# Kernel optimization log

Hardware: AMD Instinct MI355X
Metric: run time of the kernel (lower is better)

The kernel has to match this reference:

```python
import jax, jax.numpy as jnp
import numpy as np

N_NODES = 50000


def gcn_conv(x, W, b, src, dst, ew, n):
    """PyG-style GCNConv: D^-1/2 (A+I) D^-1/2 X W + b with self-loops of weight 1."""
    h = x @ W                                   # [N, out]
    loop = jnp.arange(n, dtype=src.dtype)
    s = jnp.concatenate([src, loop])            # [E+N]
    d = jnp.concatenate([dst, loop])
    w = jnp.concatenate([ew, jnp.ones((n,), dtype=x.dtype)])
    deg = jax.ops.segment_sum(w, d, num_segments=n)
    dinv = jnp.where(deg > 0, jax.lax.rsqrt(deg), 0.0)
    norm = dinv[s] * w * dinv[d]                # [E+N]
    out = jax.ops.segment_sum(h[s] * norm[:, None], d, num_segments=n)
    return out + b


def setup_inputs() -> dict:
    key = jax.random.key(0)
    ks = jax.random.split(key, 12)
    in_feats, hidden = 128, 128
    half = hidden // 2
    E = 800000
    x = jax.random.normal(ks[0], (N_NODES, in_feats), dtype=jnp.float32)
    edge_index = jax.random.randint(ks[1], (2, E), 0, N_NODES, dtype=jnp.int64)
    edge_weight = jax.random.uniform(ks[2], (E,), dtype=jnp.float32)
    def lin(k, fan_in, shape):
        bound = 1.0 / np.sqrt(fan_in)
        return jax.random.uniform(k, shape, minval=-bound, maxval=bound, dtype=jnp.float32)
    return {
        "x": x,
        "edge_index": edge_index,
        "edge_weight": edge_weight,
        "W1": lin(ks[3], in_feats, (in_feats, hidden)),
        "b1": jnp.zeros((hidden,), jnp.float32),
        "W2": lin(ks[4], hidden, (hidden, hidden)),
        "b2": jnp.zeros((hidden,), jnp.float32),
        "Ws": lin(ks[5], in_feats, (in_feats, hidden)),
        "bs": lin(ks[6], in_feats, (hidden,)),
        "Wl": lin(ks[7], in_feats, (in_feats, half)),
        "bl": jnp.zeros((half,), jnp.float32),
        "Wl2": lin(ks[8], half, (half, 1)),
        "bl2": lin(ks[9], half, (1,)),
    }


def reference(x, edge_index, edge_weight, W1, b1, W2, b2, Ws, bs, Wl, bl, Wl2, bl2):
    n = x.shape[0]
    src, dst = edge_index[0], edge_index[1]
    # conv1 + ReLU over neighbors
    h_neighbors = jax.nn.relu(gcn_conv(x, W1, b1, src, dst, edge_weight, n))
    # leader score: GCNConv -> ReLU -> Linear(.,1) -> sigmoid, per node
    ls_h = jax.nn.relu(gcn_conv(x, Wl, bl, src, dst, edge_weight, n))
    leader_score = jax.nn.sigmoid(ls_h @ Wl2 + bl2)        # [N, 1]
    # gated fusion of self projection vs neighbor aggregation
    h_self_proj = x @ Ws + bs
    h_new = (1.0 - leader_score) * h_neighbors + leader_score * h_self_proj
    h_final = jax.nn.relu(gcn_conv(h_new, W2, b2, src, dst, edge_weight, n))
    return (h_final, leader_score)
```

## Files before the change

kernel.cpp:

```cpp
#include <hip/hip_runtime.h>
#include <math.h>

#define THREADS 256
#define ELLS 96
#define GEMM_YSTRIDE 104
#define NPHA 256
#define BSHIFT 7
#define NBMAX 392
#define BCAP 2560

typedef unsigned int uint32;
typedef unsigned long long ull64;
typedef __attribute__((ext_vector_type(8))) short bf16x8;
typedef __attribute__((ext_vector_type(4))) float f32x4;
typedef __attribute__((ext_vector_type(2))) float f32x2;

__device__ __forceinline__ unsigned short f2bf_rne(float x) {
  uint32 u = __float_as_uint(x);
  u += 0x7fffu + ((u >> 16) & 1u);
  return (unsigned short)(u >> 16);
}

__device__ __forceinline__ f32x2 dw2f2(uint32 d) {
  f32x2 r;
  r.x = __uint_as_float(d << 16);
  r.y = __uint_as_float(d & 0xffff0000u);
  return r;
}


__global__ __launch_bounds__(256) void prep_fused(ull64* __restrict__ packed, uint32* __restrict__ gcnt, int n,
                                                  const float* __restrict__ W1, const float* __restrict__ Wl,
                                                  const float* __restrict__ Ws, const float* __restrict__ W2,
                                                  unsigned short* __restrict__ whi, unsigned short* __restrict__ wlo,
                                                  const float* __restrict__ x, unsigned short* __restrict__ xraw,
                                                  int nInit, int nW) {
  int b = blockIdx.x;
  int t = threadIdx.x;
  if (b < nInit) {
    int i = b * 256 + t;
    if (i < n) packed[i] = 0ull;
    if (i < NBMAX) gcnt[i] = 0u;
  } else if (b < nInit + nW) {
    int idx = (b - nInit) * 256 + t;
    if (idx >= 448 * 128) return;
    int slot = idx >> 7;
    int k = idx & 127;
    const float* W; int ncol, ncols;
    if (slot < 128)      { W = W1; ncol = slot;       ncols = 128; }
    else if (slot < 192) { W = Wl; ncol = slot - 128; ncols = 64;  }
    else if (slot < 320) { W = Ws; ncol = slot - 192; ncols = 128; }
    else                 { W = W2; ncol = slot - 320; ncols = 128; }
    float v = W[(size_t)k * ncols + ncol];
    unsigned short hi = f2bf_rne(v);
    float hif = __uint_as_float((uint32)hi << 16);
    unsigned short lo = f2bf_rne(v - hif);
    whi[idx] = hi;
    wlo[idx] = lo;
  } else {
    int i = (b - nInit - nW) * 256 + t;
    if (i >= n * 16) return;
    const float* px = x + (size_t)i * 8;
    float4 a = *(const float4*)px;
    float4 c = *(const float4*)(px + 4);
    ushort4 r0, r1;
    r0.x = f2bf_rne(a.x); r0.y = f2bf_rne(a.y); r0.z = f2bf_rne(a.z); r0.w = f2bf_rne(a.w);
    r1.x = f2bf_rne(c.x); r1.y = f2bf_rne(c.y); r1.z = f2bf_rne(c.z); r1.w = f2bf_rne(c.w);
    *(ushort4*)(xraw + (size_t)i * 8) = r0;
    *(ushort4*)(xraw + (size_t)i * 8 + 4) = r1;
  }
}


struct Chunk {
  const unsigned short* A;
  const unsigned short* whi;
  const unsigned short* wlo;
  const float* bias;
  void* out;
  int ostride;
  int obf16;
};
struct GemmArgs { Chunk c[5]; };

__device__ __forceinline__ void gemm_body(const Chunk& d, int M, int nTiles, int tile0, int tstride) {
  const unsigned short* A = d.A;
  int w = threadIdx.x >> 6, lane = threadIdx.x & 63;
  int n16 = lane & 15, quad = lane >> 4;

  bf16x8 Bh[4][4], Bl[4][4];
  {
    const unsigned short* wh = d.whi + (size_t)n16 * 128 + quad * 8;
    const unsigned short* wl = d.wlo + (size_t)n16 * 128 + quad * 8;
#pragma unroll
    for (int ct = 0; ct < 4; ct++)
#pragma unroll
      for (int ks = 0; ks < 4; ks++) {
        Bh[ct][ks] = *(const bf16x8*)(wh + ct * 16 * 128 + ks * 32);
        Bl[ct][ks] = *(const bf16x8*)(wl + ct * 16 * 128 + ks * 32);
      }
  }
  float bv[4];
#pragma unroll
  for (int ct = 0; ct < 4; ct++) bv[ct] = d.bias ? d.bias[ct * 16 + n16] : 0.f;

  int tile = tile0;
  bf16x8 av0[4], av1[4];
  if (tile < nTiles) {
    int bm = tile * 128;
    int r0 = bm + w * 32 + n16, r1 = r0 + 16;
    int r0c = r0 < M ? r0 : M - 1;
    int r1c = r1 < M ? r1 : M - 1;
    const unsigned short* a0 = A + (size_t)r0c * 128 + quad * 8;
    const unsigned short* a1 = A + (size_t)r1c * 128 + quad * 8;
#pragma unroll
    for (int ks = 0; ks < 4; ks++) {
      av0[ks] = *(const bf16x8*)(a0 + ks * 32);
      av1[ks] = *(const bf16x8*)(a1 + ks * 32);
    }
  }

  for (; tile < nTiles; tile += tstride) {
    int nxt = tile + tstride;
    bf16x8 nv0[4], nv1[4];
    if (nxt < nTiles) {
      int bm = nxt * 128;
      int r0 = bm + w * 32 + n16, r1 = r0 + 16;
      int r0c = r0 < M ? r0 : M - 1;
      int r1c = r1 < M ? r1 : M - 1;
      const unsigned short* a0 = A + (size_t)r0c * 128 + quad * 8;
      const unsigned short* a1 = A + (size_t)r1c * 128 + quad * 8;
#pragma unroll
      for (int ks = 0; ks < 4; ks++) {
        nv0[ks] = *(const bf16x8*)(a0 + ks * 32);
        nv1[ks] = *(const bf16x8*)(a1 + ks * 32);
      }
    }

    f32x4 acc[2][4];
#pragma unroll
    for (int rt = 0; rt < 2; rt++)
#pragma unroll
      for (int ct = 0; ct < 4; ct++) acc[rt][ct] = (f32x4){0.f, 0.f, 0.f, 0.f};

#pragma unroll
    for (int ks = 0; ks < 4; ks++)
#pragma unroll
      for (int ct = 0; ct < 4; ct++) {
        acc[0][ct] = __builtin_amdgcn_mfma_f32_16x16x32_bf16(av0[ks], Bh[ct][ks], acc[0][ct], 0, 0, 0);
        acc[0][ct] = __builtin_amdgcn_mfma_f32_16x16x32_bf16(av0[ks], Bl[ct][ks], acc[0][ct], 0, 0, 0);
        acc[1][ct] = __builtin_amdgcn_mfma_f32_16x16x32_bf16(av1[ks], Bh[ct][ks], acc[1][ct], 0, 0, 0);
        acc[1][ct] = __builtin_amdgcn_mfma_f32_16x16x32_bf16(av1[ks], Bl[ct][ks], acc[1][ct], 0, 0, 0);
      }

    int bm = tile * 128;
#pragma unroll
    for (int ct = 0; ct < 4; ct++) {
      int col = ct * 16 + n16;
#pragma unroll
      for (int rt = 0; rt < 2; rt++) {
#pragma unroll
        for (int reg = 0; reg < 4; reg++) {
          int row = bm + w * 32 + rt * 16 + quad * 4 + reg;
          if (row < M) {
            float v = acc[rt][ct][reg] + bv[ct];
            if (d.obf16)
              ((unsigned short*)d.out)[(size_t)row * d.ostride + col] = f2bf_rne(v);
            else
              ((float*)d.out)[(size_t)row * d.ostride + col] = v;
          }
        }
      }
    }

#pragma unroll
    for (int ks = 0; ks < 4; ks++) { av0[ks] = nv0[ks]; av1[ks] = nv1[ks]; }
  }
}

__global__ __launch_bounds__(256, 2) void gemm_v3(GemmArgs args, int M, int nTiles) {
  gemm_body(args.c[blockIdx.x], M, nTiles, blockIdx.y, gridDim.y);
}


__global__ __launch_bounds__(256, 2) void fused_sg(GemmArgs args, int M, int nTiles, int nGemm,
                                                   const int* __restrict__ ei, const float* __restrict__ ew,
                                                   uint32* __restrict__ gcnt, uint2* __restrict__ staging, int E) {
  __shared__ uint32 cntS[NBMAX], curS[NBMAX], gbS[NBMAX];
  int b = blockIdx.x;
  int gemmIdx = -1, phIdx = -1;
  int twice = NPHA * 2;
  if (b < twice) {
    if (b & 1) gemmIdx = b >> 1; else phIdx = b >> 1;
  } else {
    gemmIdx = NPHA + (b - twice);
  }

  if (phIdx >= 0) {
    int t = threadIdx.x;
    int per = (E + NPHA - 1) / NPHA;
    int start = phIdx * per;
    int end = start + per; if (end > E) end = E;
    for (int k = t; k < NBMAX; k += 256) cntS[k] = 0u;
    __syncthreads();
    for (int i = start + t; i < end; i += 256)
      atomicAdd(&cntS[(uint32)ei[E + i] >> BSHIFT], 1u);
    __syncthreads();
    for (int k = t; k < NBMAX; k += 256) {
      uint32 c = cntS[k];
      gbS[k] = c ? atomicAdd(&gcnt[k], c) : 0u;
      curS[k] = 0u;
    }
    __syncthreads();
    for (int i = start + t; i < end; i += 256) {
      int d = ei[E + i];
      int s = ei[i];
      float w = ew[i];
      int bk = d >> BSHIFT;
      uint32 pos = atomicAdd(&curS[bk], 1u) + gbS[bk];
      if (pos < BCAP)
        staging[(size_t)bk * BCAP + pos] = make_uint2(((uint32)(d & 127) << 24) | (uint32)s, __float_as_uint(w));
    }
    return;
  }

  int chunkId = gemmIdx % 5;
  int ytile = gemmIdx / 5;
  gemm_body(args.c[chunkId], M, nTiles, ytile, GEMM_YSTRIDE);
}


__global__ __launch_bounds__(256) void phaseB_kernel(const uint2* __restrict__ staging,
                                                     const uint32* __restrict__ gcnt,
                                                     ull64* __restrict__ packed, int2* __restrict__ ell,
                                                     float* __restrict__ dinv, int* __restrict__ cnt32, int n) {
  int b = blockIdx.x;
  int t = threadIdx.x;
  uint32 cnt = gcnt[b]; if (cnt > BCAP) cnt = BCAP;
  const uint2* sb = staging + (size_t)b * BCAP;
  int dbase = b << BSHIFT;
  for (uint32 i = t; i < cnt; i += 256) {
    uint2 en = sb[i];
    int d = dbase + (int)(en.x >> 24);
    int s = (int)(en.x & 0xffffffu);
    float w = __uint_as_float(en.y);
    uint32 fx = (uint32)(w * 8388608.0f + 0.5f);
    ull64 old = atomicAdd(packed + d, (1ull << 32) | (ull64)fx);
    int slot = (int)(old >> 32);
    if (slot < ELLS)
      ell[(size_t)d * ELLS + slot] = make_int2(s, __float_as_int(w));
  }
  __syncthreads();
  const float S = 1.1920928955078125e-7f;
  int dend = dbase + 128; if (dend > n) dend = n;
  for (int d = dbase + t; d < dend; d += 256) {
    ull64 p = atomicAdd(packed + d, 0ull);
    dinv[d] = rsqrtf(1.0f + (float)(uint32)(p & 0xffffffffull) * S);
    cnt32[d] = (int)(p >> 32);
  }
}


__global__ __launch_bounds__(256) void conv1_fused(const unsigned short* __restrict__ h1,
                                                   const unsigned short* __restrict__ hl,
                                                   const int* __restrict__ cnt,
                                                   const int2* __restrict__ csr,
                                                   const float* __restrict__ dinv,
                                                   const float* __restrict__ b1, const float* __restrict__ bl,
                                                   const float* __restrict__ Wl2, const float* __restrict__ bl2,
                                                   const unsigned short* __restrict__ hself,
                                                   unsigned short* __restrict__ hnew_out,
                                                   float* __restrict__ leader_out, int nnodes) {
  int wave = threadIdx.x >> 6;
  int lane = threadIdx.x & 63;
  int node = blockIdx.x * 4 + wave;
  if (node >= nnodes) return;
  int g = lane >> 4, q = lane & 15;
  bool ql = q < 8;
  int hq = q & 7;
  int rs = node * ELLS;
  int n = cnt[node];
  float di = dinv[node];
  f32x2 dv2 = {di, di};

  f32x2 acc1[4] = {};
  f32x2 accl[4] = {};
  if (g == 0) {
    uint4 v = *(const uint4*)(h1 + (size_t)node * 128 + 8 * q);
    acc1[0] = dv2 * dw2f2(v.x); acc1[1] = dv2 * dw2f2(v.y);
    acc1[2] = dv2 * dw2f2(v.z); acc1[3] = dv2 * dw2f2(v.w);
    if (ql) {
      uint4 vl = *(const uint4*)(hl + (size_t)node * 64 + 8 * q);
      accl[0] = dv2 * dw2f2(vl.x); accl[1] = dv2 * dw2f2(vl.y);
      accl[2] = dv2 * dw2f2(vl.z); accl[3] = dv2 * dw2f2(vl.w);
    }
  }

  int e = g;
  for (; e + 4 < n; e += 8) {
    int2 en0 = csr[rs + e];
    int2 en1 = csr[rs + e + 4];
    float wz0 = __int_as_float(en0.y) * dinv[en0.x];
    float wz1 = __int_as_float(en1.y) * dinv[en1.x];
    f32x2 w0 = {wz0, wz0};
    f32x2 w1 = {wz1, wz1};
    uint4 a0 = *(const uint4*)(h1 + (size_t)en0.x * 128 + 8 * q);
    uint4 a1 = *(const uint4*)(h1 + (size_t)en1.x * 128 + 8 * q);
    int srcl = ql ? en0.x : en1.x;
    float wzl = ql ? wz0 : wz1;
    uint4 c0 = *(const uint4*)(hl + (size_t)srcl * 64 + 8 * hq);
    f32x2 wl2 = {wzl, wzl};
    accl[0] += wl2 * dw2f2(c0.x);
    accl[1] += wl2 * dw2f2(c0.y);
    accl[2] += wl2 * dw2f2(c0.z);
    accl[3] += wl2 * dw2f2(c0.w);
    acc1[0] += w0 * dw2f2(a0.x) + w1 * dw2f2(a1.x);
    acc1[1] += w0 * dw2f2(a0.y) + w1 * dw2f2(a1.y);
    acc1[2] += w0 * dw2f2(a0.z) + w1 * dw2f2(a1.z);
    acc1[3] += w0 * dw2f2(a0.w) + w1 * dw2f2(a1.w);
  }
  if (e < n) {
    int2 en = csr[rs + e];
    float wz0 = __int_as_float(en.y) * dinv[en.x];
    f32x2 w0 = {wz0, wz0};
    uint4 a0 = *(const uint4*)(h1 + (size_t)en.x * 128 + 8 * q);
    float wzl = ql ? wz0 : 0.f;
    uint4 c0 = *(const uint4*)(hl + (size_t)en.x * 64 + 8 * hq);
    f32x2 wl2 = {wzl, wzl};
    accl[0] += wl2 * dw2f2(c0.x);
    accl[1] += wl2 * dw2f2(c0.y);
    accl[2] += wl2 * dw2f2(c0.z);
    accl[3] += wl2 * dw2f2(c0.w);
    acc1[0] += w0 * dw2f2(a0.x);
    acc1[1] += w0 * dw2f2(a0.y);
    acc1[2] += w0 * dw2f2(a0.z);
    acc1[3] += w0 * dw2f2(a0.w);
  }

#pragma unroll
  for (int k = 0; k < 4; k++) {
    acc1[k].x += __shfl_xor(acc1[k].x, 16);
    acc1[k].y += __shfl_xor(acc1[k].y, 16);
    acc1[k].x += __shfl_xor(acc1[k].x, 32);
    acc1[k].y += __shfl_xor(acc1[k].y, 32);
    accl[k].x += __shfl_xor(accl[k].x, 16);
    accl[k].y += __shfl_xor(accl[k].y, 16);
    accl[k].x += __shfl_xor(accl[k].x, 32);
    accl[k].y += __shfl_xor(accl[k].y, 32);
    accl[k].x += __shfl_xor(accl[k].x, 8);
    accl[k].y += __shfl_xor(accl[k].y, 8);
  }

  float part = 0.f;
  if (ql) {
    float b[8], w2[8];
    *(float4*)&b[0] = *(const float4*)(bl + 8 * q);
    *(float4*)&b[4] = *(const float4*)(bl + 8 * q + 4);
    *(float4*)&w2[0] = *(const float4*)(Wl2 + 8 * q);
    *(float4*)&w2[4] = *(const float4*)(Wl2 + 8 * q + 4);
#pragma unroll
    for (int k = 0; k < 4; k++) {
      part += fmaxf(di * accl[k].x + b[2 * k], 0.f) * w2[2 * k];
      part += fmaxf(di * accl[k].y + b[2 * k + 1], 0.f) * w2[2 * k + 1];
    }
  }
  part += __shfl_xor(part, 1);
  part += __shfl_xor(part, 2);
  part += __shfl_xor(part, 4);
  float z = __shfl(part, 0) + bl2[0];
  float l = 1.f / (1.f + expf(-z));
  if (lane == 0) leader_out[node] = l;

  if (g == 0) {
    float b[8], r[8], hs[8];
    *(float4*)&b[0] = *(const float4*)(b1 + 8 * q);
    *(float4*)&b[4] = *(const float4*)(b1 + 8 * q + 4);
    uint4 hsv = *(const uint4*)(hself + (size_t)node * 128 + 8 * q);
    f32x2 h0 = dw2f2(hsv.x), h1v = dw2f2(hsv.y), h2v = dw2f2(hsv.z), h3v = dw2f2(hsv.w);
    hs[0] = h0.x; hs[1] = h0.y; hs[2] = h1v.x; hs[3] = h1v.y;
    hs[4] = h2v.x; hs[5] = h2v.y; hs[6] = h3v.x; hs[7] = h3v.y;
    float a[8];
    a[0] = acc1[0].x; a[1] = acc1[0].y; a[2] = acc1[1].x; a[3] = acc1[1].y;
    a[4] = acc1[2].x; a[5] = acc1[2].y; a[6] = acc1[3].x; a[7] = acc1[3].y;
#pragma unroll
    for (int j = 0; j < 8; j++) {
      r[j] = fmaxf(di * a[j] + b[j], 0.f);
      r[j] = (1.f - l) * r[j] + l * hs[j];
      r[j] *= di;
    }
    ushort4 p0, p1;
    p0.x = f2bf_rne(r[0]); p0.y = f2bf_rne(r[1]); p0.z = f2bf_rne(r[2]); p0.w = f2bf_rne(r[3]);
    p1.x = f2bf_rne(r[4]); p1.y = f2bf_rne(r[5]); p1.z = f2bf_rne(r[6]); p1.w = f2bf_rne(r[7]);
    *(ushort4*)(hnew_out + (size_t)node * 128 + 8 * q) = p0;
    *(ushort4*)(hnew_out + (size_t)node * 128 + 8 * q + 4) = p1;
  }
}


__global__ __launch_bounds__(256) void agg_conv2_kernel(const unsigned short* __restrict__ h,
                                                        const int* __restrict__ cnt,
                                                        const int2* __restrict__ csr,
                                                        const float* __restrict__ dinv, const float* __restrict__ bias,
                                                        float* __restrict__ out, int nnodes) {
  int wave = threadIdx.x >> 6;
  int lane = threadIdx.x & 63;
  int node = blockIdx.x * 4 + wave;
  if (node >= nnodes) return;
  int g = lane >> 4;
  int q = lane & 15;
  int rs = node * ELLS;
  int n = cnt[node];
  float di = dinv[node];

  f32x2 acc[4] = {};
  if (g == 0) {
    uint4 v = *(const uint4*)(h + (size_t)node * 128 + 8 * q);
    acc[0] = dw2f2(v.x); acc[1] = dw2f2(v.y);
    acc[2] = dw2f2(v.z); acc[3] = dw2f2(v.w);
  }
  int e = g;
  for (; e + 4 < n; e += 8) {
    int2 en0 = csr[rs + e];
    int2 en1 = csr[rs + e + 4];
    f32x2 w0 = {__int_as_float(en0.y), __int_as_float(en0.y)};
    f32x2 w1 = {__int_as_float(en1.y), __int_as_float(en1.y)};
    uint4 v0 = *(const uint4*)(h + (size_t)en0.x * 128 + 8 * q);
    uint4 v1 = *(const uint4*)(h + (size_t)en1.x * 128 + 8 * q);
    acc[0] += w0 * dw2f2(v0.x) + w1 * dw2f2(v1.x);
    acc[1] += w0 * dw2f2(v0.y) + w1 * dw2f2(v1.y);
    acc[2] += w0 * dw2f2(v0.z) + w1 * dw2f2(v1.z);
    acc[3] += w0 * dw2f2(v0.w) + w1 * dw2f2(v1.w);
  }
  if (e < n) {
    int2 en = csr[rs + e];
    f32x2 w0 = {__int_as_float(en.y), __int_as_float(en.y)};
    uint4 v = *(const uint4*)(h + (size_t)en.x * 128 + 8 * q);
    acc[0] += w0 * dw2f2(v.x);
    acc[1] += w0 * dw2f2(v.y);
    acc[2] += w0 * dw2f2(v.z);
    acc[3] += w0 * dw2f2(v.w);
  }
#pragma unroll
  for (int k = 0; k < 4; k++) {
    acc[k].x += __shfl_xor(acc[k].x, 16);
    acc[k].y += __shfl_xor(acc[k].y, 16);
    acc[k].x += __shfl_xor(acc[k].x, 32);
    acc[k].y += __shfl_xor(acc[k].y, 32);
  }
  if (g == 0) {
    float b[8], r[8];
    *(float4*)&b[0] = *(const float4*)(bias + 8 * q);
    *(float4*)&b[4] = *(const float4*)(bias + 8 * q + 4);
    float a[8];
    a[0] = acc[0].x; a[1] = acc[0].y; a[2] = acc[1].x; a[3] = acc[1].y;
    a[4] = acc[2].x; a[5] = acc[2].y; a[6] = acc[3].x; a[7] = acc[3].y;
#pragma unroll
    for (int j = 0; j < 8; j++) r[j] = fmaxf(di * a[j] + b[j], 0.f);
    *(float4*)(out + (size_t)node * 128 + 8 * q) = *(float4*)&r[0];
    *(float4*)(out + (size_t)node * 128 + 8 * q + 4) = *(float4*)&r[4];
  }
}


extern "C" void kernel_launch(void* const* d_in, const int* in_sizes, int n_in,
                              void* d_out, int out_size, void* d_ws, size_t ws_size,
                              hipStream_t stream) {
  const float* x   = (const float*)d_in[0];
  const int*   ei  = (const int*)d_in[1];
  const float* ew  = (const float*)d_in[2];
  const float* W1  = (const float*)d_in[3];
  const float* b1  = (const float*)d_in[4];
  const float* W2  = (const float*)d_in[5];
  const float* b2  = (const float*)d_in[6];
  const float* Wsp = (const float*)d_in[7];
  const float* bs  = (const float*)d_in[8];
  const float* Wl  = (const float*)d_in[9];
  const float* bl  = (const float*)d_in[10];
  const float* Wl2 = (const float*)d_in[11];
  const float* bl2 = (const float*)d_in[12];

  const int N = in_sizes[0] / 128;
  const int E = in_sizes[1] / 2;
  const int NB = (N + 127) >> BSHIFT;

  char* ws = (char*)d_ws;
  size_t off = 0;
  auto alloc = [&](size_t bytes) -> void* {
    void* p = ws + off;
    off = (off + bytes + 255) & ~(size_t)255;
    return p;
  };
  ull64* packed    = (ull64*)alloc((size_t)N * 8);
  uint32* gcnt     = (uint32*)alloc((size_t)NBMAX * 4);
  uint2* staging   = (uint2*)alloc((size_t)NBMAX * BCAP * 8);
  float* dinv      = (float*)alloc((size_t)N * 4);
  int*   cnt32     = (int*)alloc((size_t)N * 4);
  int2*  ell       = (int2*)alloc((size_t)N * ELLS * 8);
  unsigned short* xraw   = (unsigned short*)alloc((size_t)N * 128 * 2);
  unsigned short* h1bf   = (unsigned short*)alloc((size_t)N * 128 * 2);
  unsigned short* hlbf   = (unsigned short*)alloc((size_t)N * 64 * 2);
  unsigned short* hnewbf = (unsigned short*)alloc((size_t)N * 128 * 2);
  unsigned short* hspbf  = (unsigned short*)alloc((size_t)N * 128 * 2);
  unsigned short* whi = (unsigned short*)alloc((size_t)448 * 128 * 2);
  unsigned short* wlo = (unsigned short*)alloc((size_t)448 * 128 * 2);

  float* h_final = (float*)d_out;
  float* leader  = (float*)d_out + (size_t)N * 128;

  int gN = (N + THREADS - 1) / THREADS;
  int gWave = (N + 3) / 4;
  int nTiles = (N + 127) / 128;
  int nCast = (N * 16 + 255) / 256;
  int nW = (448 * 128 + 255) / 256;

  prep_fused<<<gN + nW + nCast, 256, 0, stream>>>(packed, gcnt, N, W1, Wl, Wsp, W2, whi, wlo, x, xraw, gN, nW);

  {
    GemmArgs ga;
    ga.c[0] = {xraw, whi + 0 * 128,   wlo + 0 * 128,   nullptr, h1bf,       128, 1};
    ga.c[1] = {xraw, whi + 64 * 128,  wlo + 64 * 128,  nullptr, h1bf + 64,  128, 1};
    ga.c[2] = {xraw, whi + 128 * 128, wlo + 128 * 128, nullptr, hlbf,       64,  1};
    ga.c[3] = {xraw, whi + 192 * 128, wlo + 192 * 128, bs,      hspbf,      128, 1};
    ga.c[4] = {xraw, whi + 256 * 128, wlo + 256 * 128, bs + 64, hspbf + 64, 128, 1};
    int nGemm = 5 * GEMM_YSTRIDE;
    int totalBlocks = NPHA * 2 + (nGemm - NPHA);
    fused_sg<<<totalBlocks, 256, 0, stream>>>(ga, N, nTiles, nGemm, ei, ew, gcnt, staging, E);
  }

  phaseB_kernel<<<NB, 256, 0, stream>>>(staging, gcnt, packed, ell, dinv, cnt32, N);

  conv1_fused<<<gWave, 256, 0, stream>>>(h1bf, hlbf, cnt32, ell, dinv,
                                         b1, bl, Wl2, bl2, hspbf, hnewbf, leader, N);

  {
    GemmArgs ga;
    ga.c[0] = {hnewbf, whi + 320 * 128, wlo + 320 * 128, nullptr, h1bf,      128, 1};
    ga.c[1] = {hnewbf, whi + 384 * 128, wlo + 384 * 128, nullptr, h1bf + 64, 128, 1};
    ga.c[2] = ga.c[0]; ga.c[3] = ga.c[0]; ga.c[4] = ga.c[0];
    gemm_v3<<<dim3(2, 256), 256, 0, stream>>>(ga, N, nTiles);
  }
  agg_conv2_kernel<<<gWave, 256, 0, stream>>>(h1bf, cnt32, ell,
                                              dinv, b2, h_final, N);
}
```

Measured before the change: 267.9 us.

## Fold input/weight bf16 conversion into GEMMs and use shared-memory degree accumulation

Removes the prep kernel. The GEMM now reads fp32 x directly and converts it to bf16 in registers, and each block builds its bf16 hi/lo weight split itself from the fp32 weights. The phaseB degree and count accumulation moves from global 64-bit atomics on a packed array to per-block shared-memory atomics, and a small memset replaces the rest of the zero-init. This saves one launch and the xraw round trip. In exchange the GEMM reads twice as many bytes for A, and every block does strided scalar weight loads and conversions.

```diff
diff --git a/kernel.cpp b/kernel.cpp
--- a/kernel.cpp
+++ b/kernel.cpp
@@ -28,77 +28,47 @@
   return r;
 }
 
-
-__global__ __launch_bounds__(256) void prep_fused(ull64* __restrict__ packed, uint32* __restrict__ gcnt, int n,
-                                                  const float* __restrict__ W1, const float* __restrict__ Wl,
-                                                  const float* __restrict__ Ws, const float* __restrict__ W2,
-                                                  unsigned short* __restrict__ whi, unsigned short* __restrict__ wlo,
-                                                  const float* __restrict__ x, unsigned short* __restrict__ xraw,
-                                                  int nInit, int nW) {
-  int b = blockIdx.x;
-  int t = threadIdx.x;
-  if (b < nInit) {
-    int i = b * 256 + t;
-    if (i < n) packed[i] = 0ull;
-    if (i < NBMAX) gcnt[i] = 0u;
-  } else if (b < nInit + nW) {
-    int idx = (b - nInit) * 256 + t;
-    if (idx >= 448 * 128) return;
-    int slot = idx >> 7;
-    int k = idx & 127;
-    const float* W; int ncol, ncols;
-    if (slot < 128)      { W = W1; ncol = slot;       ncols = 128; }
-    else if (slot < 192) { W = Wl; ncol = slot - 128; ncols = 64;  }
-    else if (slot < 320) { W = Ws; ncol = slot - 192; ncols = 128; }
-    else                 { W = W2; ncol = slot - 320; ncols = 128; }
-    float v = W[(size_t)k * ncols + ncol];
-    unsigned short hi = f2bf_rne(v);
-    float hif = __uint_as_float((uint32)hi << 16);
-    unsigned short lo = f2bf_rne(v - hif);
-    whi[idx] = hi;
-    wlo[idx] = lo;
-  } else {
-    int i = (b - nInit - nW) * 256 + t;
-    if (i >= n * 16) return;
-    const float* px = x + (size_t)i * 8;
-    float4 a = *(const float4*)px;
-    float4 c = *(const float4*)(px + 4);
-    ushort4 r0, r1;
-    r0.x = f2bf_rne(a.x); r0.y = f2bf_rne(a.y); r0.z = f2bf_rne(a.z); r0.w = f2bf_rne(a.w);
-    r1.x = f2bf_rne(c.x); r1.y = f2bf_rne(c.y); r1.z = f2bf_rne(c.z); r1.w = f2bf_rne(c.w);
-    *(ushort4*)(xraw + (size_t)i * 8) = r0;
-    *(ushort4*)(xraw + (size_t)i * 8 + 4) = r1;
-  }
+__device__ __forceinline__ bf16x8 cvt8(float4 a, float4 b) {
+  bf16x8 r;
+  r[0] = (short)f2bf_rne(a.x); r[1] = (short)f2bf_rne(a.y);
+  r[2] = (short)f2bf_rne(a.z); r[3] = (short)f2bf_rne(a.w);
+  r[4] = (short)f2bf_rne(b.x); r[5] = (short)f2bf_rne(b.y);
+  r[6] = (short)f2bf_rne(b.z); r[7] = (short)f2bf_rne(b.w);
+  return r;
 }
 
 
 struct Chunk {
-  const unsigned short* A;
-  const unsigned short* whi;
-  const unsigned short* wlo;
+  const void* A;
+  const float* W;
+  int wcols;
+  int colbase;
   const float* bias;
   void* out;
   int ostride;
-  int obf16;
 };
 struct GemmArgs { Chunk c[5]; };
 
+template <bool AF32>
 __device__ __forceinline__ void gemm_body(const Chunk& d, int M, int nTiles, int tile0, int tstride) {
-  const unsigned short* A = d.A;
   int w = threadIdx.x >> 6, lane = threadIdx.x & 63;
   int n16 = lane & 15, quad = lane >> 4;
 
   bf16x8 Bh[4][4], Bl[4][4];
   {
-    const unsigned short* wh = d.whi + (size_t)n16 * 128 + quad * 8;
-    const unsigned short* wl = d.wlo + (size_t)n16 * 128 + quad * 8;
+    const float* wb = d.W + d.colbase + n16;
 #pragma unroll
     for (int ct = 0; ct < 4; ct++)
 #pragma unroll
-      for (int ks = 0; ks < 4; ks++) {
-        Bh[ct][ks] = *(const bf16x8*)(wh + ct * 16 * 128 + ks * 32);
-        Bl[ct][ks] = *(const bf16x8*)(wl + ct * 16 * 128 + ks * 32);
-      }
+      for (int ks = 0; ks < 4; ks++)
+#pragma unroll
+        for (int j = 0; j < 8; j++) {
+          float v = wb[(size_t)(quad * 8 + ks * 32 + j) * d.wcols + ct * 16];
+          unsigned short hi = f2bf_rne(v);
+          float hif = __uint_as_float((uint32)hi << 16);
+          Bh[ct][ks][j] = (short)hi;
+          Bl[ct][ks][j] = (short)f2bf_rne(v - hif);
+        }
   }
   float bv[4];
 #pragma unroll
@@ -111,29 +81,53 @@
     int r0 = bm + w * 32 + n16, r1 = r0 + 16;
     int r0c = r0 < M ? r0 : M - 1;
     int r1c = r1 < M ? r1 : M - 1;
-    const unsigned short* a0 = A + (size_t)r0c * 128 + quad * 8;
-    const unsigned short* a1 = A + (size_t)r1c * 128 + quad * 8;
-#pragma unroll
-    for (int ks = 0; ks < 4; ks++) {
-      av0[ks] = *(const bf16x8*)(a0 + ks * 32);
-      av1[ks] = *(const bf16x8*)(a1 + ks * 32);
+    if constexpr (AF32) {
+      const float* a0 = (const float*)d.A + (size_t)r0c * 128 + quad * 8;
+      const float* a1 = (const float*)d.A + (size_t)r1c * 128 + quad * 8;
+#pragma unroll
+      for (int ks = 0; ks < 4; ks++) {
+        av0[ks] = cvt8(*(const float4*)(a0 + ks * 32), *(const float4*)(a0 + ks * 32 + 4));
+        av1[ks] = cvt8(*(const float4*)(a1 + ks * 32), *(const float4*)(a1 + ks * 32 + 4));
+      }
+    } else {
+      const unsigned short* a0 = (const unsigned short*)d.A + (size_t)r0c * 128 + quad * 8;
+      const unsigned short* a1 = (const unsigned short*)d.A + (size_t)r1c * 128 + quad * 8;
+#pragma unroll
+      for (int ks = 0; ks < 4; ks++) {
+        av0[ks] = *(const bf16x8*)(a0 + ks * 32);
+        av1[ks] = *(const bf16x8*)(a1 + ks * 32);
+      }
     }
   }
 
   for (; tile < nTiles; tile += tstride) {
     int nxt = tile + tstride;
+    bool have = (nxt < nTiles);
+    float4 pf0[8], pf1[8];
     bf16x8 nv0[4], nv1[4];
-    if (nxt < nTiles) {
+    if (have) {
       int bm = nxt * 128;
       int r0 = bm + w * 32 + n16, r1 = r0 + 16;
       int r0c = r0 < M ? r0 : M - 1;
       int r1c = r1 < M ? r1 : M - 1;
-      const unsigned short* a0 = A + (size_t)r0c * 128 + quad * 8;
-      const unsigned short* a1 = A + (size_t)r1c * 128 + quad * 8;
-#pragma unroll
-      for (int ks = 0; ks < 4; ks++) {
-        nv0[ks] = *(const bf16x8*)(a0 + ks * 32);
-        nv1[ks] = *(const bf16x8*)(a1 + ks * 32);
+      if constexpr (AF32) {
+        const float* a0 = (const float*)d.A + (size_t)r0c * 128 + quad * 8;
+        const float* a1 = (const float*)d.A + (size_t)r1c * 128 + quad * 8;
+#pragma unroll
+        for (int ks = 0; ks < 4; ks++) {
+          pf0[2 * ks]     = *(const float4*)(a0 + ks * 32);
+          pf0[2 * ks + 1] = *(const float4*)(a0 + ks * 32 + 4);
+          pf1[2 * ks]     = *(const float4*)(a1 + ks * 32);
+          pf1[2 * ks + 1] = *(const float4*)(a1 + ks * 32 + 4);
+        }
+      } else {
+        const unsigned short* a0 = (const unsigned short*)d.A + (size_t)r0c * 128 + quad * 8;
+        const unsigned short* a1 = (const unsigned short*)d.A + (size_t)r1c * 128 + quad * 8;
+#pragma unroll
+        for (int ks = 0; ks < 4; ks++) {
+          nv0[ks] = *(const bf16x8*)(a0 + ks * 32);
+          nv1[ks] = *(const bf16x8*)(a1 + ks * 32);
+        }
       }
     }
 
@@ -164,22 +158,29 @@
           int row = bm + w * 32 + rt * 16 + quad * 4 + reg;
           if (row < M) {
             float v = acc[rt][ct][reg] + bv[ct];
-            if (d.obf16)
-              ((unsigned short*)d.out)[(size_t)row * d.ostride + col] = f2bf_rne(v);
-            else
-              ((float*)d.out)[(size_t)row * d.ostride + col] = v;
+            ((unsigned short*)d.out)[(size_t)row * d.ostride + col] = f2bf_rne(v);
           }
         }
       }
     }
 
-#pragma unroll
-    for (int ks = 0; ks < 4; ks++) { av0[ks] = nv0[ks]; av1[ks] = nv1[ks]; }
+    if (have) {
+      if constexpr (AF32) {
+#pragma unroll
+        for (int ks = 0; ks < 4; ks++) {
+          av0[ks] = cvt8(pf0[2 * ks], pf0[2 * ks + 1]);
+          av1[ks] = cvt8(pf1[2 * ks], pf1[2 * ks + 1]);
+        }
+      } else {
+#pragma unroll
+        for (int ks = 0; ks < 4; ks++) { av0[ks] = nv0[ks]; av1[ks] = nv1[ks]; }
+      }
+    }
   }
 }
 
 __global__ __launch_bounds__(256, 2) void gemm_v3(GemmArgs args, int M, int nTiles) {
-  gemm_body(args.c[blockIdx.x], M, nTiles, blockIdx.y, gridDim.y);
+  gemm_body<false>(args.c[blockIdx.x], M, nTiles, blockIdx.y, gridDim.y);
 }
 
 
@@ -226,37 +227,42 @@
 
   int chunkId = gemmIdx % 5;
   int ytile = gemmIdx / 5;
-  gemm_body(args.c[chunkId], M, nTiles, ytile, GEMM_YSTRIDE);
+  gemm_body<true>(args.c[chunkId], M, nTiles, ytile, GEMM_YSTRIDE);
 }
 
 
 __global__ __launch_bounds__(256) void phaseB_kernel(const uint2* __restrict__ staging,
                                                      const uint32* __restrict__ gcnt,
-                                                     ull64* __restrict__ packed, int2* __restrict__ ell,
+                                                     int2* __restrict__ ell,
                                                      float* __restrict__ dinv, int* __restrict__ cnt32, int n) {
+  __shared__ uint32 cntL[128], sumL[128];
   int b = blockIdx.x;
   int t = threadIdx.x;
+  if (t < 128) { cntL[t] = 0u; sumL[t] = 0u; }
+  __syncthreads();
   uint32 cnt = gcnt[b]; if (cnt > BCAP) cnt = BCAP;
   const uint2* sb = staging + (size_t)b * BCAP;
   int dbase = b << BSHIFT;
   for (uint32 i = t; i < cnt; i += 256) {
     uint2 en = sb[i];
-    int d = dbase + (int)(en.x >> 24);
+    int dl = (int)(en.x >> 24);
     int s = (int)(en.x & 0xffffffu);
     float w = __uint_as_float(en.y);
     uint32 fx = (uint32)(w * 8388608.0f + 0.5f);
-    ull64 old = atomicAdd(packed + d, (1ull << 32) | (ull64)fx);
-    int slot = (int)(old >> 32);
+    atomicAdd(&sumL[dl], fx);
+    uint32 slot = atomicAdd(&cntL[dl], 1u);
     if (slot < ELLS)
-      ell[(size_t)d * ELLS + slot] = make_int2(s, __float_as_int(w));
+      ell[(size_t)(dbase + dl) * ELLS + slot] = make_int2(s, __float_as_int(w));
   }
   __syncthreads();
-  const float S = 1.1920928955078125e-7f;
-  int dend = dbase + 128; if (dend > n) dend = n;
-  for (int d = dbase + t; d < dend; d += 256) {
-    ull64 p = atomicAdd(packed + d, 0ull);
-    dinv[d] = rsqrtf(1.0f + (float)(uint32)(p & 0xffffffffull) * S);
-    cnt32[d] = (int)(p >> 32);
+  if (t < 128) {
+    int d = dbase + t;
+    if (d < n) {
+      const float S = 1.1920928955078125e-7f;
+      dinv[d] = rsqrtf(1.0f + (float)sumL[t] * S);
+      uint32 c = cntL[t];
+      cnt32[d] = (int)(c < ELLS ? c : ELLS);
+    }
   }
 }
 
@@ -490,52 +496,45 @@
     off = (off + bytes + 255) & ~(size_t)255;
     return p;
   };
-  ull64* packed    = (ull64*)alloc((size_t)N * 8);
   uint32* gcnt     = (uint32*)alloc((size_t)NBMAX * 4);
   uint2* staging   = (uint2*)alloc((size_t)NBMAX * BCAP * 8);
   float* dinv      = (float*)alloc((size_t)N * 4);
   int*   cnt32     = (int*)alloc((size_t)N * 4);
   int2*  ell       = (int2*)alloc((size_t)N * ELLS * 8);
-  unsigned short* xraw   = (unsigned short*)alloc((size_t)N * 128 * 2);
   unsigned short* h1bf   = (unsigned short*)alloc((size_t)N * 128 * 2);
   unsigned short* hlbf   = (unsigned short*)alloc((size_t)N * 64 * 2);
   unsigned short* hnewbf = (unsigned short*)alloc((size_t)N * 128 * 2);
   unsigned short* hspbf  = (unsigned short*)alloc((size_t)N * 128 * 2);
-  unsigned short* whi = (unsigned short*)alloc((size_t)448 * 128 * 2);
-  unsigned short* wlo = (unsigned short*)alloc((size_t)448 * 128 * 2);
 
   float* h_final = (float*)d_out;
   float* leader  = (float*)d_out + (size_t)N * 128;
 
-  int gN = (N + THREADS - 1) / THREADS;
   int gWave = (N + 3) / 4;
   int nTiles = (N + 127) / 128;
-  int nCast = (N * 16 + 255) / 256;
-  int nW = (448 * 128 + 255) / 256;
-
-  prep_fused<<<gN + nW + nCast, 256, 0, stream>>>(packed, gcnt, N, W1, Wl, Wsp, W2, whi, wlo, x, xraw, gN, nW);
+
+  hipMemsetAsync(gcnt, 0, (size_t)NBMAX * 4, stream);
 
   {
     GemmArgs ga;
-    ga.c[0] = {xraw, whi + 0 * 128,   wlo + 0 * 128,   nullptr, h1bf,       128, 1};
-    ga.c[1] = {xraw, whi + 64 * 128,  wlo + 64 * 128,  nullptr, h1bf + 64,  128, 1};
-    ga.c[2] = {xraw, whi + 128 * 128, wlo + 128 * 128, nullptr, hlbf,       64,  1};
-    ga.c[3] = {xraw, whi + 192 * 128, wlo + 192 * 128, bs,      hspbf,      128, 1};
-    ga.c[4] = {xraw, whi + 256 * 128, wlo + 256 * 128, bs + 64, hspbf + 64, 128, 1};
+    ga.c[0] = {x, W1,  128, 0,  nullptr, h1bf,       128};
+    ga.c[1] = {x, W1,  128, 64, nullptr, h1bf + 64,  128};
+    ga.c[2] = {x, Wl,  64,  0,  nullptr, hlbf,       64};
+    ga.c[3] = {x, Wsp, 128, 0,  bs,      hspbf,      128};
+    ga.c[4] = {x, Wsp, 128, 64, bs + 64, hspbf + 64, 128};
     int nGemm = 5 * GEMM_YSTRIDE;
     int totalBlocks = NPHA * 2 + (nGemm - NPHA);
     fused_sg<<<totalBlocks, 256, 0, stream>>>(ga, N, nTiles, nGemm, ei, ew, gcnt, staging, E);
   }
 
-  phaseB_kernel<<<NB, 256, 0, stream>>>(staging, gcnt, packed, ell, dinv, cnt32, N);
+  phaseB_kernel<<<NB, 256, 0, stream>>>(staging, gcnt, ell, dinv, cnt32, N);
 
   conv1_fused<<<gWave, 256, 0, stream>>>(h1bf, hlbf, cnt32, ell, dinv,
                                          b1, bl, Wl2, bl2, hspbf, hnewbf, leader, N);
 
   {
     GemmArgs ga;
-    ga.c[0] = {hnewbf, whi + 320 * 128, wlo + 320 * 128, nullptr, h1bf,      128, 1};
-    ga.c[1] = {hnewbf, whi + 384 * 128, wlo + 384 * 128, nullptr, h1bf + 64, 128, 1};
+    ga.c[0] = {hnewbf, W2, 128, 0,  nullptr, h1bf,      128};
+    ga.c[1] = {hnewbf, W2, 128, 64, nullptr, h1bf + 64, 128};
     ga.c[2] = ga.c[0]; ga.c[3] = ga.c[0]; ga.c[4] = ga.c[0];
     gemm_v3<<<dim3(2, 256), 256, 0, stream>>>(ga, N, nTiles);
   }
```

Measured after the change: 301.0 us. +12.4%, slower.

## Sort scatter entries in LDS before staging write and use LDS atomics in phase B

Applied to the files above, without the earlier changes.

The bucketing phase now counts edges per bucket, pads each bucket count to a multiple of 8, prefix-sums the padded counts, and sorts edges into shared memory. It then writes them to staging in contiguous 8-entry lines, with sentinel entries filling the padding, instead of issuing scattered global writes. Phase B drops the global 64-bit packed atomics and accumulates per-destination count and weight sum with shared-memory atomics, which removes the packed array and its zero-init. The costs are a large LDS footprint in a kernel that shares blocks with the GEMM, which may lower occupancy, plus extra sentinel entries that phase B must skip.

```diff
diff --git a/kernel.cpp b/kernel.cpp
--- a/kernel.cpp
+++ b/kernel.cpp
@@ -7,7 +7,10 @@
 #define NPHA 256
 #define BSHIFT 7
 #define NBMAX 392
-#define BCAP 2560
+#define BCAP 4096
+#define PERMAX 3136
+#define PMAX 5872
+#define LMAX 736
 
 typedef unsigned int uint32;
 typedef unsigned long long ull64;
@@ -29,20 +32,20 @@
 }
 
 
-__global__ __launch_bounds__(256) void prep_fused(ull64* __restrict__ packed, uint32* __restrict__ gcnt, int n,
+__global__ __launch_bounds__(256) void prep_fused(uint32* __restrict__ gcnt, int n,
                                                   const float* __restrict__ W1, const float* __restrict__ Wl,
                                                   const float* __restrict__ Ws, const float* __restrict__ W2,
                                                   unsigned short* __restrict__ whi, unsigned short* __restrict__ wlo,
                                                   const float* __restrict__ x, unsigned short* __restrict__ xraw,
-                                                  int nInit, int nW) {
+                                                  int nW) {
   int b = blockIdx.x;
   int t = threadIdx.x;
-  if (b < nInit) {
-    int i = b * 256 + t;
-    if (i < n) packed[i] = 0ull;
-    if (i < NBMAX) gcnt[i] = 0u;
-  } else if (b < nInit + nW) {
-    int idx = (b - nInit) * 256 + t;
+  if (b == 0) {
+    for (int k = t; k < NBMAX; k += 256) gcnt[k] = 0u;
+  }
+  if (b < 1 + nW) {
+    if (b == 0) return;
+    int idx = (b - 1) * 256 + t;
     if (idx >= 448 * 128) return;
     int slot = idx >> 7;
     int k = idx & 127;
@@ -58,7 +61,7 @@
     whi[idx] = hi;
     wlo[idx] = lo;
   } else {
-    int i = (b - nInit - nW) * 256 + t;
+    int i = (b - 1 - nW) * 256 + t;
     if (i >= n * 16) return;
     const float* px = x + (size_t)i * 8;
     float4 a = *(const float4*)px;
@@ -186,7 +189,11 @@
 __global__ __launch_bounds__(256, 2) void fused_sg(GemmArgs args, int M, int nTiles, int nGemm,
                                                    const int* __restrict__ ei, const float* __restrict__ ew,
                                                    uint32* __restrict__ gcnt, uint2* __restrict__ staging, int E) {
-  __shared__ uint32 cntS[NBMAX], curS[NBMAX], gbS[NBMAX];
+  __shared__ uint32 cntS[NBMAX], offS[NBMAX], gbS[NBMAX], curS[NBMAX];
+  __shared__ unsigned short lineBk[LMAX];
+  __shared__ uint2 sortedS[PMAX];
+  __shared__ uint32 Ptot;
+
   int b = blockIdx.x;
   int gemmIdx = -1, phIdx = -1;
   int twice = NPHA * 2;
@@ -206,20 +213,47 @@
     for (int i = start + t; i < end; i += 256)
       atomicAdd(&cntS[(uint32)ei[E + i] >> BSHIFT], 1u);
     __syncthreads();
+    if (t < 64) {
+      uint32 carry = 0;
+      for (int base = 0; base < NBMAX; base += 64) {
+        int k = base + t;
+        uint32 v = (k < NBMAX) ? ((cntS[k] + 7u) & ~7u) : 0u;
+        uint32 s = v;
+#pragma unroll
+        for (int dd = 1; dd < 64; dd <<= 1) {
+          uint32 o = __shfl_up(s, dd);
+          if (t >= dd) s += o;
+        }
+        if (k < NBMAX) offS[k] = carry + s - v;
+        carry += __shfl(s, 63);
+      }
+      if (t == 0) Ptot = carry;
+    }
+    __syncthreads();
+    uint32 P = Ptot;
     for (int k = t; k < NBMAX; k += 256) {
-      uint32 c = cntS[k];
-      gbS[k] = c ? atomicAdd(&gcnt[k], c) : 0u;
+      uint32 pc = (cntS[k] + 7u) & ~7u;
+      gbS[k] = pc ? atomicAdd(&gcnt[k], pc) : 0u;
       curS[k] = 0u;
-    }
+      uint32 l1 = (offS[k] + pc) >> 3;
+      for (uint32 l = offS[k] >> 3; l < l1; l++) lineBk[l] = (unsigned short)k;
+    }
+    for (uint32 j = t; j < P; j += 256) sortedS[j] = make_uint2(0xFFFFFFFFu, 0u);
     __syncthreads();
     for (int i = start + t; i < end; i += 256) {
       int d = ei[E + i];
       int s = ei[i];
       float w = ew[i];
       int bk = d >> BSHIFT;
-      uint32 pos = atomicAdd(&curS[bk], 1u) + gbS[bk];
-      if (pos < BCAP)
-        staging[(size_t)bk * BCAP + pos] = make_uint2(((uint32)(d & 127) << 24) | (uint32)s, __float_as_uint(w));
+      uint32 pos = offS[bk] + atomicAdd(&curS[bk], 1u);
+      sortedS[pos] = make_uint2(((uint32)(d & 127) << 24) | (uint32)s, __float_as_uint(w));
+    }
+    __syncthreads();
+    for (uint32 j = t; j < P; j += 256) {
+      int k = lineBk[j >> 3];
+      uint32 idx = gbS[k] + (j - offS[k]);
+      if (idx < BCAP)
+        staging[(size_t)k * BCAP + idx] = sortedS[j];
     }
     return;
   }
@@ -232,31 +266,37 @@
 
 __global__ __launch_bounds__(256) void phaseB_kernel(const uint2* __restrict__ staging,
                                                      const uint32* __restrict__ gcnt,
-                                                     ull64* __restrict__ packed, int2* __restrict__ ell,
+                                                     int2* __restrict__ ell,
                                                      float* __restrict__ dinv, int* __restrict__ cnt32, int n) {
+  __shared__ uint32 cntL[128], sumL[128];
   int b = blockIdx.x;
   int t = threadIdx.x;
+  if (t < 128) { cntL[t] = 0u; sumL[t] = 0u; }
+  __syncthreads();
   uint32 cnt = gcnt[b]; if (cnt > BCAP) cnt = BCAP;
   const uint2* sb = staging + (size_t)b * BCAP;
   int dbase = b << BSHIFT;
   for (uint32 i = t; i < cnt; i += 256) {
     uint2 en = sb[i];
-    int d = dbase + (int)(en.x >> 24);
+    if ((en.x >> 24) == 0xFFu) continue;
+    int dl = (int)(en.x >> 24);
     int s = (int)(en.x & 0xffffffu);
     float w = __uint_as_float(en.y);
     uint32 fx = (uint32)(w * 8388608.0f + 0.5f);
-    ull64 old = atomicAdd(packed + d, (1ull << 32) | (ull64)fx);
-    int slot = (int)(old >> 32);
+    atomicAdd(&sumL[dl], fx);
+    uint32 slot = atomicAdd(&cntL[dl], 1u);
     if (slot < ELLS)
-      ell[(size_t)d * ELLS + slot] = make_int2(s, __float_as_int(w));
+      ell[(size_t)(dbase + dl) * ELLS + slot] = make_int2(s, __float_as_int(w));
   }
   __syncthreads();
-  const float S = 1.1920928955078125e-7f;
-  int dend = dbase + 128; if (dend > n) dend = n;
-  for (int d = dbase + t; d < dend; d += 256) {
-    ull64 p = atomicAdd(packed + d, 0ull);
-    dinv[d] = rsqrtf(1.0f + (float)(uint32)(p & 0xffffffffull) * S);
-    cnt32[d] = (int)(p >> 32);
+  if (t < 128) {
+    int d = dbase + t;
+    if (d < n) {
+      const float S = 1.1920928955078125e-7f;
+      dinv[d] = rsqrtf(1.0f + (float)sumL[t] * S);
+      uint32 c = cntL[t];
+      cnt32[d] = (int)(c < ELLS ? c : ELLS);
+    }
   }
 }
 
@@ -490,7 +530,6 @@
     off = (off + bytes + 255) & ~(size_t)255;
     return p;
   };
-  ull64* packed    = (ull64*)alloc((size_t)N * 8);
   uint32* gcnt     = (uint32*)alloc((size_t)NBMAX * 4);
   uint2* staging   = (uint2*)alloc((size_t)NBMAX * BCAP * 8);
   float* dinv      = (float*)alloc((size_t)N * 4);
@@ -507,13 +546,12 @@
   float* h_final = (float*)d_out;
   float* leader  = (float*)d_out + (size_t)N * 128;
 
-  int gN = (N + THREADS - 1) / THREADS;
   int gWave = (N + 3) / 4;
   int nTiles = (N + 127) / 128;
   int nCast = (N * 16 + 255) / 256;
   int nW = (448 * 128 + 255) / 256;
 
-  prep_fused<<<gN + nW + nCast, 256, 0, stream>>>(packed, gcnt, N, W1, Wl, Wsp, W2, whi, wlo, x, xraw, gN, nW);
+  prep_fused<<<1 + nW + nCast, 256, 0, stream>>>(gcnt, N, W1, Wl, Wsp, W2, whi, wlo, x, xraw, nW);
 
   {
     GemmArgs ga;
@@ -527,7 +565,7 @@
     fused_sg<<<totalBlocks, 256, 0, stream>>>(ga, N, nTiles, nGemm, ei, ew, gcnt, staging, E);
   }
 
-  phaseB_kernel<<<NB, 256, 0, stream>>>(staging, gcnt, packed, ell, dinv, cnt32, N);
+  phaseB_kernel<<<NB, 256, 0, stream>>>(staging, gcnt, ell, dinv, cnt32, N);
 
   conv1_fused<<<gWave, 256, 0, stream>>>(h1bf, hlbf, cnt32, ell, dinv,
                                          b1, bl, Wl2, bl2, hspbf, hnewbf, leader, N);
```

After: 254.0 us. 5.2% less time.
